# Optimization experiments

Measured on AMD Instinct MI355X. Metric: run time of the kernel, lower is better.

The kernel has to match this reference:

```python
import jax, jax.numpy as jnp
import numpy as np

B, N = 8, 16384
NPOINT, RADIUS, NSAMPLE, IN_CH = 512, 0.5, 64, 6
EPS = 1e-5


def _sqdist(a, b):
    # a [B,S,3], b [B,N,3] -> [B,S,N] squared euclidean distances
    return (jnp.sum(a * a, -1)[:, :, None] + jnp.sum(b * b, -1)[:, None, :]
            - 2.0 * jnp.einsum('bsd,bnd->bsn', a, b))


def _fps(xyz, npoint):
    # farthest point sampling (deterministic: starts from index 0)
    Bb, Nn, _ = xyz.shape
    def body(carry, _):
        dist, far = carry  # dist [B,N], far [B]
        centroid = jnp.take_along_axis(xyz, far[:, None, None], axis=1)  # [B,1,3]
        d = jnp.sum((xyz - centroid) ** 2, -1)
        dist = jnp.minimum(dist, d)
        return (dist, jnp.argmax(dist, -1).astype(jnp.int32)), far
    init = (jnp.full((Bb, Nn), 1e10, xyz.dtype), jnp.zeros((Bb,), jnp.int32))
    _, idx = jax.lax.scan(body, init, None, length=npoint)
    return idx.T  # [B, npoint]


def _ball_query(radius, nsample, xyz, new_xyz):
    Nn = xyz.shape[1]
    sq = _sqdist(new_xyz, xyz)  # [B,S,N]
    gidx = jnp.where(sq > radius * radius, Nn,
                     jnp.arange(Nn, dtype=jnp.int32)[None, None, :])
    gidx = jnp.sort(gidx, axis=-1)[:, :, :nsample]  # [B,S,K]
    # pad slots (==N) get the first valid index, as in reference torch code
    return jnp.where(gidx == Nn, gidx[:, :, :1], gidx)


def _gather(x, idx):
    # x [B,N,C], idx [B,...] -> [B,...,C]
    return jax.vmap(lambda xb, ib: xb[ib])(x, idx)


def _forward(xyz, points, layers):
    fps_idx = _fps(xyz, NPOINT)
    new_xyz = _gather(xyz, fps_idx)                        # [B,S,3]
    idx = _ball_query(RADIUS, NSAMPLE, xyz, new_xyz)       # [B,S,K]
    grouped_xyz = _gather(xyz, idx) - new_xyz[:, :, None]  # [B,S,K,3]
    grouped_pts = _gather(points, idx)                     # [B,S,K,3]
    h = jnp.concatenate([grouped_xyz, grouped_pts], -1)[..., :IN_CH]  # [B,S,K,6]
    for (W, b, g, beta) in layers:
        # 1x1 Conv2d == per-point linear; BatchNorm2d (train mode) over (B,K,S)
        h = jnp.einsum('bskc,oc->bsko', h, W) + b
        mu = jnp.mean(h, axis=(0, 1, 2))
        var = jnp.var(h, axis=(0, 1, 2))
        h = jax.nn.relu(g * (h - mu) * jax.lax.rsqrt(var + EPS) + beta)
    return new_xyz, jnp.max(h, axis=2)  # [B,S,3], [B,S,C_out]


def setup_inputs() -> dict:
    key = jax.random.key(0)
    ks = jax.random.split(key, 4)
    return {
        'xyz': jax.random.normal(ks[0], (B, N, 3), jnp.float32),
        'points': jax.random.normal(ks[1], (B, N, 3), jnp.float32),
        'W0': jax.random.normal(ks[2], (64, IN_CH), jnp.float32) * (1.0 / np.sqrt(IN_CH)),
        'b0': jnp.zeros((64,), jnp.float32),
        'g0': jnp.ones((64,), jnp.float32),
        'beta0': jnp.zeros((64,), jnp.float32),
        'W1': jax.random.normal(ks[3], (128, 64), jnp.float32) * (1.0 / np.sqrt(64)),
        'b1': jnp.zeros((128,), jnp.float32),
        'g1': jnp.ones((128,), jnp.float32),
        'beta1': jnp.zeros((128,), jnp.float32),
    }


def reference(xyz, points, W0, b0, g0, beta0, W1, b1, g1, beta1):
    layers = [(W0, b0, g0, beta0), (W1, b1, g1, beta1)]
    return _forward(xyz, points, layers)
```

## Files before the change

### kernel.cpp

```cpp
#include <hip/hip_runtime.h>

#define NB    8
#define NPTS  16384
#define NS    512
#define NK    64
#define C1    64
#define C2    128
#define RAD2  0.25f
#define MTOT  (NB*NS*NK)

typedef float v2f __attribute__((ext_vector_type(2)));
typedef __bf16 bfv8 __attribute__((ext_vector_type(8)));
typedef float f32x4 __attribute__((ext_vector_type(4)));

extern __shared__ char dynsmem[];

#define UMAX_DPP(x, CTRL, RM)                                                   \
    do {                                                                        \
        unsigned _m = (unsigned)__builtin_amdgcn_update_dpp((int)(x), (int)(x), \
                                                            CTRL, RM, 0xf, false); \
        x = (x > _m) ? x : _m;                                                  \
    } while (0)
#define UMIN_DPP(x, CTRL, RM)                                                   \
    do {                                                                        \
        unsigned _m = (unsigned)__builtin_amdgcn_update_dpp((int)(x), (int)(x), \
                                                            CTRL, RM, 0xf, false); \
        x = (x < _m) ? x : _m;                                                  \
    } while (0)
#define FSUM_DPP(x, CTRL, RM)                                                   \
    do {                                                                        \
        int _b = __builtin_amdgcn_update_dpp(0, __float_as_int(x), CTRL, RM,    \
                                             0xf, false);                       \
        x += __int_as_float(_b);                                                \
    } while (0)

__global__ __launch_bounds__(1024, 4) void fps_kernel(const float* __restrict__ xyz,
                                                      float* __restrict__ out) {
#pragma clang fp contract(off)
    int b = blockIdx.x;
    int tid = threadIdx.x;
    int lane = tid & 63;
    int w = tid >> 6;
    const float* base = xyz + (size_t)b * NPTS * 3;
    v2f* yv = (v2f*)dynsmem;
    v2f* zv = yv + 8192;
    __shared__ unsigned svals[2][16];
    __shared__ unsigned sidxs[2][16];
    v2f pxp[8], ddp[8];
#pragma unroll
    for (int jj = 0; jj < 8; ++jj) {
        int p0 = tid + (jj << 11);
        int p1 = p0 + 1024;
        float x0 = base[p0 * 3 + 0], y0 = base[p0 * 3 + 1], z0 = base[p0 * 3 + 2];
        float x1 = base[p1 * 3 + 0], y1 = base[p1 * 3 + 1], z1 = base[p1 * 3 + 2];
        pxp[jj].x = x0; pxp[jj].y = x1;
        v2f yp; yp.x = y0; yp.y = y1;
        v2f zp; zp.x = z0; zp.y = z1;
        yv[(jj << 10) + tid] = yp;
        zv[(jj << 10) + tid] = zp;
        ddp[jj].x = 1e10f; ddp[jj].y = 1e10f;
    }
    float cx = base[0], cy = base[1], cz = base[2];
    if (tid == 0) {
        float* o = out + (size_t)b * NS * 3;
        o[0] = cx; o[1] = cy; o[2] = cz;
    }
    __syncthreads();
    for (int i = 1; i < NS; ++i) {
        v2f cx2; cx2.x = cx; cx2.y = cx;
        v2f cy2; cy2.x = cy; cy2.y = cy;
        v2f cz2; cz2.x = cz; cz2.y = cz;
        v2f cm0, cm1, cm2, cm3;
        cm0.x = -1.f; cm0.y = -1.f; cm1 = cm0; cm2 = cm0; cm3 = cm0;
#pragma unroll
        for (int jj = 0; jj < 8; ++jj) {
            v2f yp = yv[(jj << 10) + tid];
            v2f zp = zv[(jj << 10) + tid];
            v2f dx = pxp[jj] - cx2;
            v2f dy = yp - cy2;
            v2f dz = zp - cz2;
            v2f d = (dx * dx + dy * dy) + dz * dz;
            v2f nd;
            nd.x = fminf(ddp[jj].x, d.x);
            nd.y = fminf(ddp[jj].y, d.y);
            ddp[jj] = nd;
            if ((jj & 3) == 0) { cm0.x = fmaxf(cm0.x, nd.x); cm0.y = fmaxf(cm0.y, nd.y); }
            if ((jj & 3) == 1) { cm1.x = fmaxf(cm1.x, nd.x); cm1.y = fmaxf(cm1.y, nd.y); }
            if ((jj & 3) == 2) { cm2.x = fmaxf(cm2.x, nd.x); cm2.y = fmaxf(cm2.y, nd.y); }
            if ((jj & 3) == 3) { cm3.x = fmaxf(cm3.x, nd.x); cm3.y = fmaxf(cm3.y, nd.y); }
        }
        v2f m01; m01.x = fmaxf(cm0.x, cm1.x); m01.y = fmaxf(cm0.y, cm1.y);
        v2f m23; m23.x = fmaxf(cm2.x, cm3.x); m23.y = fmaxf(cm2.y, cm3.y);
        float bv = fmaxf(fmaxf(m01.x, m23.x), fmaxf(m01.y, m23.y));
        unsigned vb = (unsigned)__float_as_int(bv);
        UMAX_DPP(vb, 0xB1, 0xf);
        UMAX_DPP(vb, 0x4E, 0xf);
        UMAX_DPP(vb, 0x141, 0xf);
        UMAX_DPP(vb, 0x140, 0xf);
        UMAX_DPP(vb, 0x142, 0xa);
        UMAX_DPP(vb, 0x143, 0xc);
        if (lane == 63) svals[i & 1][w] = vb;
        __syncthreads();
        unsigned wv = svals[i & 1][lane & 15];
        UMAX_DPP(wv, 0xB1, 0xf);
        UMAX_DPP(wv, 0x4E, 0xf);
        UMAX_DPP(wv, 0x141, 0xf);
        UMAX_DPP(wv, 0x140, 0xf);
        float W = __int_as_float((int)wv);
        unsigned lidx = 0x7fffffffu;
        if (__any(bv == W)) {
#pragma unroll
            for (int jj = 7; jj >= 0; --jj) {
                if (ddp[jj].y == W) lidx = (unsigned)(tid + (jj << 11) + 1024);
                if (ddp[jj].x == W) lidx = (unsigned)(tid + (jj << 11));
            }
        }
        UMIN_DPP(lidx, 0xB1, 0xf);
        UMIN_DPP(lidx, 0x4E, 0xf);
        UMIN_DPP(lidx, 0x141, 0xf);
        UMIN_DPP(lidx, 0x140, 0xf);
        UMIN_DPP(lidx, 0x142, 0xa);
        UMIN_DPP(lidx, 0x143, 0xc);
        if (lane == 63) sidxs[i & 1][w] = lidx;
        __syncthreads();
        unsigned ci = sidxs[i & 1][lane & 15];
        UMIN_DPP(ci, 0xB1, 0xf);
        UMIN_DPP(ci, 0x4E, 0xf);
        UMIN_DPP(ci, 0x141, 0xf);
        UMIN_DPP(ci, 0x140, 0xf);
        int ii = __builtin_amdgcn_readfirstlane((int)ci);
        const float* cp = base + (size_t)ii * 3;
        cx = cp[0]; cy = cp[1]; cz = cp[2];
        if (tid == 0) {
            float* o = out + ((size_t)b * NS + i) * 3;
            o[0] = cx; o[1] = cy; o[2] = cz;
        }
    }
}

__global__ __launch_bounds__(256) void ballq_kernel(const float* __restrict__ xyz,
                                                    const float* __restrict__ pts,
                                                    const float* __restrict__ newxyz,
                                                    float* __restrict__ feat,
                                                    float* __restrict__ stats) {
    int w = threadIdx.x >> 6;
    int lane = threadIdx.x & 63;
    int wid = blockIdx.x * 4 + w;
    int b = wid >> 9;
    const float* nx = newxyz + (size_t)wid * 3;
    float cx = nx[0], cy = nx[1], cz = nx[2];
    float sa = __fadd_rn(__fadd_rn(__fmul_rn(cx, cx), __fmul_rn(cy, cy)),
                         __fmul_rn(cz, cz));
    __shared__ int sidx[4][64];
    __shared__ float pm[4][27];
    const float* base = xyz + (size_t)b * NPTS * 3;
    int cnt = 0;
    for (int off = 0; off < NPTS && cnt < NK; off += 64) {
        int p = off + lane;
        float bx = base[p * 3 + 0], by = base[p * 3 + 1], bz = base[p * 3 + 2];
        float sb = __fadd_rn(__fadd_rn(__fmul_rn(bx, bx), __fmul_rn(by, by)),
                             __fmul_rn(bz, bz));
        float dt = __fadd_rn(__fadd_rn(__fmul_rn(cx, bx), __fmul_rn(cy, by)),
                             __fmul_rn(cz, bz));
        float sq = __fsub_rn(__fadd_rn(sa, sb), __fmul_rn(2.0f, dt));
        bool inb = !(sq > RAD2);
        unsigned long long mask = __ballot(inb);
        int pos = cnt + (int)__popcll(mask & ((1ull << lane) - 1ull));
        if (inb && pos < NK) sidx[w][pos] = p;
        cnt += (int)__popcll(mask);
    }
    __syncthreads();
    int filled = cnt < NK ? cnt : NK;
    int sel = (lane < filled) ? lane : 0;
    int p = (filled > 0) ? sidx[w][sel] : 0;
    float gx = base[p * 3 + 0], gy = base[p * 3 + 1], gz = base[p * 3 + 2];
    const float* pb = pts + (size_t)b * NPTS * 3;
    float rowf[6];
    rowf[0] = __fsub_rn(gx, cx);
    rowf[1] = __fsub_rn(gy, cy);
    rowf[2] = __fsub_rn(gz, cz);
    rowf[3] = pb[p * 3 + 0];
    rowf[4] = pb[p * 3 + 1];
    rowf[5] = pb[p * 3 + 2];
    float* fr = feat + ((size_t)wid * NK + lane) * 6;
#pragma unroll
    for (int j = 0; j < 6; ++j) fr[j] = rowf[j];
    float mom[27];
#pragma unroll
    for (int j = 0; j < 6; ++j) mom[j] = rowf[j];
    {
        int t = 6;
#pragma unroll
        for (int j = 0; j < 6; ++j)
#pragma unroll
            for (int k = j; k < 6; ++k) mom[t++] = rowf[j] * rowf[k];
    }
#pragma unroll
    for (int t = 0; t < 27; ++t) {
        FSUM_DPP(mom[t], 0xB1, 0xf);
        FSUM_DPP(mom[t], 0x4E, 0xf);
        FSUM_DPP(mom[t], 0x141, 0xf);
        FSUM_DPP(mom[t], 0x140, 0xf);
        FSUM_DPP(mom[t], 0x142, 0xa);
        FSUM_DPP(mom[t], 0x143, 0xc);
        if (lane == 63) pm[w][t] = mom[t];
    }
    __syncthreads();
    if (threadIdx.x < 27) {
        int t = threadIdx.x;
        float s = pm[0][t] + pm[1][t] + pm[2][t] + pm[3][t];
        atomicAdd(&stats[t], s);
    }
}

__device__ __forceinline__ void bf16_split(float v, unsigned short& hi, unsigned short& lo) {
    unsigned u = __float_as_uint(v);
    unsigned h = (u + 0x7fffu + ((u >> 16) & 1u)) >> 16;
    float rem = v - __uint_as_float(h << 16);
    unsigned ur = __float_as_uint(rem);
    unsigned l = (ur + 0x7fffu + ((ur >> 16) & 1u)) >> 16;
    hi = (unsigned short)h; lo = (unsigned short)l;
}

__device__ __forceinline__ void bn0_from_moments(const float* __restrict__ stats,
                                                 const float* __restrict__ g0,
                                                 const float* __restrict__ be0,
                                                 const float* w0r, float b0v,
                                                 int lane, float& a0, float& c0v) {
    const float inv = 1.0f / (float)MTOT;
    float m6[6];
#pragma unroll
    for (int j = 0; j < 6; ++j) m6[j] = stats[j];
    float s = 0.f;
#pragma unroll
    for (int j = 0; j < 6; ++j) s = fmaf(w0r[j], m6[j], s);
    float quad = 0.f;
    {
        int t = 6;
#pragma unroll
        for (int j = 0; j < 6; ++j)
#pragma unroll
            for (int k = j; k < 6; ++k) {
                float coef = w0r[j] * w0r[k];
                if (j != k) coef = coef + coef;
                quad = fmaf(coef, stats[t], quad);
                ++t;
            }
    }
    float mu0 = fmaf(s, inv, b0v);
    float e2 = fmaf(quad, inv, fmaf(2.f * b0v * s, inv, b0v * b0v));
    float var0 = fmaxf(e2 - mu0 * mu0, 0.f);
    a0 = g0[lane] * rsqrtf(var0 + 1e-5f);
    c0v = fmaf(-mu0, a0, be0[lane]);
}

__global__ __launch_bounds__(256) void stats1_mfma_kernel(const float* __restrict__ feat,
                                                          const float* __restrict__ W0,
                                                          const float* __restrict__ b0,
                                                          const float* __restrict__ W1,
                                                          const float* __restrict__ b1,
                                                          const float* __restrict__ g0,
                                                          const float* __restrict__ be0,
                                                          float* __restrict__ stats) {
    char* lds = dynsmem;
    int tid = threadIdx.x;
    int lane = tid & 63;
    int w = tid >> 6;
    int g = blockIdx.x * 4 + w;
    for (int idx = tid; idx < 8192; idx += 256) {
        int o = idx >> 6, c = idx & 63;
        unsigned short hi, lo;
        bf16_split(W1[idx], hi, lo);
        int byt = (c * 2) ^ ((o & 7) << 4);
        *(unsigned short*)(lds + o * 128 + byt) = hi;
        *(unsigned short*)(lds + 16384 + o * 128 + byt) = lo;
    }
    float w0r[6];
#pragma unroll
    for (int j = 0; j < 6; ++j) w0r[j] = W0[lane * 6 + j];
    float b0v = b0[lane];
    float a0, c0v;
    bn0_from_moments(stats, g0, be0, w0r, b0v, lane, a0, c0v);
    char* X = lds + 32768 + w * 16384;
    __syncthreads();
    const float* fb = feat + (size_t)g * 64 * 6;
#pragma unroll 4
    for (int r = 0; r < 64; ++r) {
        const float* f = fb + r * 6;
        float h = b0v;
#pragma unroll
        for (int j = 0; j < 6; ++j) h = fmaf(w0r[j], f[j], h);
        float hn = fmaxf(fmaf(a0, h, c0v), 0.f);
        unsigned short hi, lo;
        bf16_split(hn, hi, lo);
        int byt = (lane * 2) ^ ((r & 7) << 4);
        *(unsigned short*)(X + r * 128 + byt) = hi;
        *(unsigned short*)(X + 8192 + r * 128 + byt) = lo;
    }
    __syncthreads();
    float b1v[8];
#pragma unroll
    for (int tn = 0; tn < 8; ++tn) b1v[tn] = b1[tn * 16 + (lane & 15)];
    float ssum[8], ssq[8];
#pragma unroll
    for (int tn = 0; tn < 8; ++tn) { ssum[tn] = 0.f; ssq[tn] = 0.f; }
#pragma unroll
    for (int tm = 0; tm < 4; ++tm) {
        bfv8 Ah[2], Al[2];
#pragma unroll
        for (int tk = 0; tk < 2; ++tk) {
            int r = tm * 16 + (lane & 15);
            int colb = (((lane >> 4) * 16) + tk * 64) ^ ((r & 7) << 4);
            Ah[tk] = *(const bfv8*)(X + r * 128 + colb);
            Al[tk] = *(const bfv8*)(X + 8192 + r * 128 + colb);
        }
#pragma unroll
        for (int tn = 0; tn < 8; ++tn) {
            int o = tn * 16 + (lane & 15);
            f32x4 acc = {0.f, 0.f, 0.f, 0.f};
#pragma unroll
            for (int tk = 0; tk < 2; ++tk) {
                int colb = (((lane >> 4) * 16) + tk * 64) ^ ((o & 7) << 4);
                bfv8 Bh = *(const bfv8*)(lds + o * 128 + colb);
                bfv8 Bl = *(const bfv8*)(lds + 16384 + o * 128 + colb);
                acc = __builtin_amdgcn_mfma_f32_16x16x32_bf16(Ah[tk], Bh, acc, 0, 0, 0);
                acc = __builtin_amdgcn_mfma_f32_16x16x32_bf16(Ah[tk], Bl, acc, 0, 0, 0);
                acc = __builtin_amdgcn_mfma_f32_16x16x32_bf16(Al[tk], Bh, acc, 0, 0, 0);
            }
#pragma unroll
            for (int j = 0; j < 4; ++j) {
                float h1 = acc[j] + b1v[tn];
                ssum[tn] += h1;
                ssq[tn] = fmaf(h1, h1, ssq[tn]);
            }
        }
    }
#pragma unroll
    for (int tn = 0; tn < 8; ++tn) {
        ssum[tn] += __shfl_xor(ssum[tn], 16);
        ssum[tn] += __shfl_xor(ssum[tn], 32);
        ssq[tn] += __shfl_xor(ssq[tn], 16);
        ssq[tn] += __shfl_xor(ssq[tn], 32);
    }
    __syncthreads();
    float* psum = (float*)(lds + 32768);
    float* psq  = (float*)(lds + 32768 + 4096);
    if (lane < 16) {
#pragma unroll
        for (int tn = 0; tn < 8; ++tn) {
            psum[w * 256 + tn * 16 + lane] = ssum[tn];
            psq[w * 256 + tn * 16 + lane] = ssq[tn];
        }
    }
    __syncthreads();
    if (tid < 128) {
        int ch = tid;
        float s = psum[ch] + psum[256 + ch] + psum[512 + ch] + psum[768 + ch];
        float q = psq[ch] + psq[256 + ch] + psq[512 + ch] + psq[768 + ch];
        atomicAdd(&stats[128 + ch], s);
        atomicAdd(&stats[256 + ch], q);
    }
}

__global__ __launch_bounds__(256) void final_mfma_kernel(const float* __restrict__ feat,
                                                         const float* __restrict__ W0,
                                                         const float* __restrict__ b0,
                                                         const float* __restrict__ W1,
                                                         const float* __restrict__ b1,
                                                         const float* __restrict__ g0,
                                                         const float* __restrict__ be0,
                                                         const float* __restrict__ g1,
                                                         const float* __restrict__ be1,
                                                         const float* __restrict__ stats,
                                                         float* __restrict__ out) {
    char* lds = dynsmem;
    int tid = threadIdx.x;
    int lane = tid & 63;
    int w = tid >> 6;
    int g = blockIdx.x * 4 + w;
    for (int idx = tid; idx < 8192; idx += 256) {
        int o = idx >> 6, c = idx & 63;
        unsigned short hi, lo;
        bf16_split(W1[idx], hi, lo);
        int byt = (c * 2) ^ ((o & 7) << 4);
        *(unsigned short*)(lds + o * 128 + byt) = hi;
        *(unsigned short*)(lds + 16384 + o * 128 + byt) = lo;
    }
    float w0r[6];
#pragma unroll
    for (int j = 0; j < 6; ++j) w0r[j] = W0[lane * 6 + j];
    float b0v = b0[lane];
    float a0, c0v;
    bn0_from_moments(stats, g0, be0, w0r, b0v, lane, a0, c0v);
    char* X = lds + 32768 + w * 16384;
    __syncthreads();
    const float* fb = feat + (size_t)g * 64 * 6;
#pragma unroll 4
    for (int r = 0; r < 64; ++r) {
        const float* f = fb + r * 6;
        float h = b0v;
#pragma unroll
        for (int j = 0; j < 6; ++j) h = fmaf(w0r[j], f[j], h);
        float hn = fmaxf(fmaf(a0, h, c0v), 0.f);
        unsigned short hi, lo;
        bf16_split(hn, hi, lo);
        int byt = (lane * 2) ^ ((r & 7) << 4);
        *(unsigned short*)(X + r * 128 + byt) = hi;
        *(unsigned short*)(X + 8192 + r * 128 + byt) = lo;
    }
    __syncthreads();
    const float inv = 1.0f / (float)MTOT;
    float a1v[8], d1v[8];
#pragma unroll
    for (int tn = 0; tn < 8; ++tn) {
        int o = tn * 16 + (lane & 15);
        float mu1 = stats[128 + o] * inv;
        float var1 = fmaxf(stats[256 + o] * inv - mu1 * mu1, 0.f);
        float a1 = g1[o] * rsqrtf(var1 + 1e-5f);
        float c1 = fmaf(-mu1, a1, be1[o]);
        a1v[tn] = a1;
        d1v[tn] = fmaf(a1, b1[o], c1);
    }
    float mx[8];
#pragma unroll
    for (int tn = 0; tn < 8; ++tn) mx[tn] = -1e30f;
#pragma unroll
    for (int tm = 0; tm < 4; ++tm) {
        bfv8 Ah[2], Al[2];
#pragma unroll
        for (int tk = 0; tk < 2; ++tk) {
            int r = tm * 16 + (lane & 15);
            int colb = (((lane >> 4) * 16) + tk * 64) ^ ((r & 7) << 4);
            Ah[tk] = *(const bfv8*)(X + r * 128 + colb);
            Al[tk] = *(const bfv8*)(X + 8192 + r * 128 + colb);
        }
#pragma unroll
        for (int tn = 0; tn < 8; ++tn) {
            int o = tn * 16 + (lane & 15);
            f32x4 acc = {0.f, 0.f, 0.f, 0.f};
#pragma unroll
            for (int tk = 0; tk < 2; ++tk) {
                int colb = (((lane >> 4) * 16) + tk * 64) ^ ((o & 7) << 4);
                bfv8 Bh = *(const bfv8*)(lds + o * 128 + colb);
                bfv8 Bl = *(const bfv8*)(lds + 16384 + o * 128 + colb);
                acc = __builtin_amdgcn_mfma_f32_16x16x32_bf16(Ah[tk], Bh, acc, 0, 0, 0);
                acc = __builtin_amdgcn_mfma_f32_16x16x32_bf16(Ah[tk], Bl, acc, 0, 0, 0);
                acc = __builtin_amdgcn_mfma_f32_16x16x32_bf16(Al[tk], Bh, acc, 0, 0, 0);
            }
            float t0 = fmaxf(fmaf(a1v[tn], acc[0], d1v[tn]), 0.f);
            float t1 = fmaxf(fmaf(a1v[tn], acc[1], d1v[tn]), 0.f);
            float t2 = fmaxf(fmaf(a1v[tn], acc[2], d1v[tn]), 0.f);
            float t3 = fmaxf(fmaf(a1v[tn], acc[3], d1v[tn]), 0.f);
            mx[tn] = fmaxf(mx[tn], fmaxf(fmaxf(t0, t1), fmaxf(t2, t3)));
        }
    }
#pragma unroll
    for (int tn = 0; tn < 8; ++tn) {
        float v = mx[tn];
        v = fmaxf(v, __shfl_xor(v, 16));
        v = fmaxf(v, __shfl_xor(v, 32));
        mx[tn] = v;
    }
    if (lane < 16) {
        size_t ob = 12288 + (size_t)g * 128;
#pragma unroll
        for (int tn = 0; tn < 8; ++tn) out[ob + tn * 16 + lane] = mx[tn];
    }
}

extern "C" void kernel_launch(void* const* d_in, const int* in_sizes, int n_in,
                              void* d_out, int out_size, void* d_ws, size_t ws_size,
                              hipStream_t stream) {
    const float* xyz = (const float*)d_in[0];
    const float* pts = (const float*)d_in[1];
    const float* W0  = (const float*)d_in[2];
    const float* b0  = (const float*)d_in[3];
    const float* g0  = (const float*)d_in[4];
    const float* be0 = (const float*)d_in[5];
    const float* W1  = (const float*)d_in[6];
    const float* b1  = (const float*)d_in[7];
    const float* g1  = (const float*)d_in[8];
    const float* be1 = (const float*)d_in[9];
    float* out = (float*)d_out;

    float* feat  = (float*)d_ws;
    float* stats = feat + (size_t)MTOT * 6;

    const int fps_lds = 2 * NPTS * (int)sizeof(float);
    (void)hipFuncSetAttribute(reinterpret_cast<const void*>(fps_kernel),
                              hipFuncAttributeMaxDynamicSharedMemorySize, fps_lds);
    const int fm_lds = 98304;
    (void)hipFuncSetAttribute(reinterpret_cast<const void*>(stats1_mfma_kernel),
                              hipFuncAttributeMaxDynamicSharedMemorySize, fm_lds);
    (void)hipFuncSetAttribute(reinterpret_cast<const void*>(final_mfma_kernel),
                              hipFuncAttributeMaxDynamicSharedMemorySize, fm_lds);

    (void)hipMemsetAsync(stats, 0, 384 * sizeof(float), stream);
    fps_kernel<<<NB, 1024, fps_lds, stream>>>(xyz, out);
    ballq_kernel<<<1024, 256, 0, stream>>>(xyz, pts, out, feat, stats);
    stats1_mfma_kernel<<<1024, 256, fm_lds, stream>>>(feat, W0, b0, W1, b1, g0, be0, stats);
    final_mfma_kernel<<<1024, 256, fm_lds, stream>>>(feat, W0, b0, W1, b1, g0, be0, g1, be1, stats, out);
}
```

Before: 991.5 us.

## Keep FPS point coordinates in registers and fold stats memset into FPS kernel

The FPS kernel now holds all y/z coordinates in per-thread registers instead of re-reading them from LDS on each of the 511 serial iterations. The stats zeroing moves from a separate hipMemsetAsync into the FPS kernel, removing one launch. The index min-reduction is moved inside the any-match branch so waves with no candidate skip it. This raises register pressure on a 1024-thread block, which could cause spills.

```diff
diff --git a/kernel.cpp b/kernel.cpp
--- a/kernel.cpp
+++ b/kernel.cpp
@@ -34,30 +34,26 @@
         x += __int_as_float(_b);                                                \
     } while (0)
 
-__global__ __launch_bounds__(1024, 4) void fps_kernel(const float* __restrict__ xyz,
-                                                      float* __restrict__ out) {
+__global__ __launch_bounds__(1024, 4)
+void fps_kernel(const float* __restrict__ xyz, float* __restrict__ out,
+                float* __restrict__ stats) {
 #pragma clang fp contract(off)
     int b = blockIdx.x;
     int tid = threadIdx.x;
     int lane = tid & 63;
     int w = tid >> 6;
+    if (b == 0 && tid < 384) stats[tid] = 0.f;
     const float* base = xyz + (size_t)b * NPTS * 3;
-    v2f* yv = (v2f*)dynsmem;
-    v2f* zv = yv + 8192;
     __shared__ unsigned svals[2][16];
     __shared__ unsigned sidxs[2][16];
-    v2f pxp[8], ddp[8];
+    v2f pxp[8], pyp[8], pzp[8], ddp[8];
 #pragma unroll
     for (int jj = 0; jj < 8; ++jj) {
         int p0 = tid + (jj << 11);
         int p1 = p0 + 1024;
-        float x0 = base[p0 * 3 + 0], y0 = base[p0 * 3 + 1], z0 = base[p0 * 3 + 2];
-        float x1 = base[p1 * 3 + 0], y1 = base[p1 * 3 + 1], z1 = base[p1 * 3 + 2];
-        pxp[jj].x = x0; pxp[jj].y = x1;
-        v2f yp; yp.x = y0; yp.y = y1;
-        v2f zp; zp.x = z0; zp.y = z1;
-        yv[(jj << 10) + tid] = yp;
-        zv[(jj << 10) + tid] = zp;
+        pxp[jj].x = base[p0 * 3 + 0]; pxp[jj].y = base[p1 * 3 + 0];
+        pyp[jj].x = base[p0 * 3 + 1]; pyp[jj].y = base[p1 * 3 + 1];
+        pzp[jj].x = base[p0 * 3 + 2]; pzp[jj].y = base[p1 * 3 + 2];
         ddp[jj].x = 1e10f; ddp[jj].y = 1e10f;
     }
     float cx = base[0], cy = base[1], cz = base[2];
@@ -74,11 +70,9 @@
         cm0.x = -1.f; cm0.y = -1.f; cm1 = cm0; cm2 = cm0; cm3 = cm0;
 #pragma unroll
         for (int jj = 0; jj < 8; ++jj) {
-            v2f yp = yv[(jj << 10) + tid];
-            v2f zp = zv[(jj << 10) + tid];
             v2f dx = pxp[jj] - cx2;
-            v2f dy = yp - cy2;
-            v2f dz = zp - cz2;
+            v2f dy = pyp[jj] - cy2;
+            v2f dz = pzp[jj] - cz2;
             v2f d = (dx * dx + dy * dy) + dz * dz;
             v2f nd;
             nd.x = fminf(ddp[jj].x, d.x);
@@ -114,13 +108,13 @@
                 if (ddp[jj].y == W) lidx = (unsigned)(tid + (jj << 11) + 1024);
                 if (ddp[jj].x == W) lidx = (unsigned)(tid + (jj << 11));
             }
-        }
-        UMIN_DPP(lidx, 0xB1, 0xf);
-        UMIN_DPP(lidx, 0x4E, 0xf);
-        UMIN_DPP(lidx, 0x141, 0xf);
-        UMIN_DPP(lidx, 0x140, 0xf);
-        UMIN_DPP(lidx, 0x142, 0xa);
-        UMIN_DPP(lidx, 0x143, 0xc);
+            UMIN_DPP(lidx, 0xB1, 0xf);
+            UMIN_DPP(lidx, 0x4E, 0xf);
+            UMIN_DPP(lidx, 0x141, 0xf);
+            UMIN_DPP(lidx, 0x140, 0xf);
+            UMIN_DPP(lidx, 0x142, 0xa);
+            UMIN_DPP(lidx, 0x143, 0xc);
+        }
         if (lane == 63) sidxs[i & 1][w] = lidx;
         __syncthreads();
         unsigned ci = sidxs[i & 1][lane & 15];
@@ -486,17 +480,13 @@
     float* feat  = (float*)d_ws;
     float* stats = feat + (size_t)MTOT * 6;
 
-    const int fps_lds = 2 * NPTS * (int)sizeof(float);
-    (void)hipFuncSetAttribute(reinterpret_cast<const void*>(fps_kernel),
-                              hipFuncAttributeMaxDynamicSharedMemorySize, fps_lds);
     const int fm_lds = 98304;
     (void)hipFuncSetAttribute(reinterpret_cast<const void*>(stats1_mfma_kernel),
                               hipFuncAttributeMaxDynamicSharedMemorySize, fm_lds);
     (void)hipFuncSetAttribute(reinterpret_cast<const void*>(final_mfma_kernel),
                               hipFuncAttributeMaxDynamicSharedMemorySize, fm_lds);
 
-    (void)hipMemsetAsync(stats, 0, 384 * sizeof(float), stream);
-    fps_kernel<<<NB, 1024, fps_lds, stream>>>(xyz, out);
+    fps_kernel<<<NB, 1024, 0, stream>>>(xyz, out, stats);
     ballq_kernel<<<1024, 256, 0, stream>>>(xyz, pts, out, feat, stats);
     stats1_mfma_kernel<<<1024, 256, fm_lds, stream>>>(feat, W0, b0, W1, b1, g0, be0, stats);
     final_mfma_kernel<<<1024, 256, fm_lds, stream>>>(feat, W0, b0, W1, b1, g0, be0, g1, be1, stats, out);
```

Measured after the change: 932.3 us. -6.0%, faster.
